# Optimization experiments

Hardware: AMD Instinct MI355X
Metric: run time of the kernel (lower is better)

## Reference

```python
import jax, jax.numpy as jnp
import numpy as np
from jax import lax

F_SIZE = 128
N_HEADS = 8
HEAD_D = F_SIZE // N_HEADS
LANE_F = 64
NUM_PREDS = 6


def _layernorm(x, g, b, eps=1e-5):
    m = x.mean(-1, keepdims=True)
    v = jnp.var(x, axis=-1, keepdims=True)
    return (x - m) * lax.rsqrt(v + eps) * g + b


def _lstm_cell(x, h, c, wih, whh, bih, bhh):
    # PyTorch LSTMCell: gates ordered i, f, g, o
    gates = x @ wih.T + bih + h @ whh.T + bhh
    i, f, g, o = jnp.split(gates, 4, axis=-1)
    c2 = jax.nn.sigmoid(f) * c + jax.nn.sigmoid(i) * jnp.tanh(g)
    h2 = jax.nn.sigmoid(o) * jnp.tanh(c2)
    return h2, c2


def _to_xy(dl, yaw):
    return jnp.concatenate([dl * jnp.cos(yaw), dl * jnp.sin(yaw)], axis=-1)


def _attention(tok_pos, h_ego, h, lane_tok, key_mask, wq, wk, wv, wo, pos_w, pos_b):
    # tokens = [ego, vehicles], keys/values = [tokens, lanes]
    B = h_ego.shape[0]
    tok = jnp.concatenate([h_ego, h], axis=1) + tok_pos @ pos_w + pos_b  # [B,N1,F]
    kv = jnp.concatenate([tok, lane_tok], axis=1)  # [B,N1+L,F]
    q = (tok @ wq).reshape(B, -1, N_HEADS, HEAD_D)
    k = (kv @ wk).reshape(B, -1, N_HEADS, HEAD_D)
    v = (kv @ wv).reshape(B, -1, N_HEADS, HEAD_D)
    s = jnp.einsum('bqhd,bkhd->bhqk', q, k) / jnp.asarray(np.sqrt(HEAD_D), jnp.float32)
    s = jnp.where(key_mask[:, None, None, :] > 0, s, -1e9)
    a = jax.nn.softmax(s, axis=-1)
    o = jnp.einsum('bhqk,bkhd->bqhd', a, v).reshape(B, -1, F_SIZE) @ wo
    tok = tok + o
    return tok[:, :1], tok[:, 1:]


def _forward(input, init_pos, lane_input, mask_input, lane_mask,
             conv_w, conv_b, pos_w, pos_b,
             lane_w1, lane_b1, lane_w2, lane_b2, lane_to_f,
             wq, wk, wv, wo, ln_ego_g, ln_ego_b, ln_g, ln_b,
             ego_wih, ego_whh, ego_bih, ego_bhh,
             veh_wih, veh_whh, veh_bih, veh_bhh,
             out_ego_w, out_ego_b, out_w, out_b, len_pred):
    T, B, N1, _ = input.shape
    V = N1 - 1
    Hh = T - 2  # valid conv over time with kernel 3

    # shared conv_input applied to ego+vehicles at once (same weights in original)
    x = jnp.transpose(input, (1, 3, 2, 0))  # [B,2,N1,T]
    feat = lax.conv_general_dilated(x, conv_w, (1, 1), 'VALID',
                                    dimension_numbers=('NCHW', 'OIHW', 'NCHW'))
    feat = feat + conv_b[None, :, None, None]
    feat = jnp.transpose(feat, (3, 0, 2, 1))  # [Hh,B,N1,F]
    h_ego_seq, h_seq = feat[:, :, :1], feat[:, :, 1:]

    # lane embedding: per-point MLP + mean pool
    lanes = jax.nn.relu(lane_input @ lane_w1 + lane_b1)
    lanes = jax.nn.relu(lanes @ lane_w2 + lane_b2).mean(axis=2)  # [B,L,LANE_F]
    lane_tok = lanes @ lane_to_f  # [B,L,F]
    key_mask = jnp.concatenate([mask_input, lane_mask], axis=1)  # [B,N1+L]

    pos0 = init_pos[0]
    pe0, pv0 = pos0[:, :1], pos0[:, 1:]

    def cell_step(hx_ego, cx_ego, hx, cx, he, hv, pe, pv):
        tok_pos = jnp.concatenate([pe, pv], axis=1)
        ae, av = _attention(tok_pos, he, hv, lane_tok, key_mask, wq, wk, wv, wo, pos_w, pos_b)
        ae = _layernorm(ae.reshape(B, F_SIZE), ln_ego_g, ln_ego_b)
        av = _layernorm(av.reshape(B * V, F_SIZE), ln_g, ln_b)
        hx_ego, cx_ego = _lstm_cell(ae, hx_ego, cx_ego, ego_wih, ego_whh, ego_bih, ego_bhh)
        hx, cx = _lstm_cell(av, hx, cx, veh_wih, veh_whh, veh_bih, veh_bhh)
        return hx_ego, cx_ego, hx, cx

    def hist_step(carry, xs):
        hx_ego, cx_ego, hx, cx, pe, pv = carry
        he, hv, xe, xv = xs
        pe = pe + _to_xy(xe[..., 0:1], xe[..., 1:2])
        pv = pv + _to_xy(xv[..., 0:1], xv[..., 1:2])
        hx_ego, cx_ego, hx, cx = cell_step(hx_ego, cx_ego, hx, cx, he, hv, pe, pv)
        return (hx_ego, cx_ego, hx, cx, pe, pv), None

    carry0 = (jnp.zeros((B, F_SIZE)), jnp.zeros((B, F_SIZE)),
              jnp.zeros((B * V, F_SIZE)), jnp.zeros((B * V, F_SIZE)), pe0, pv0)
    xs = (h_ego_seq, h_seq, input[:Hh, :, :1, :].transpose(0, 1, 2, 3), input[:Hh, :, 1:, :])
    carry, _ = lax.scan(hist_step, carry0, xs)
    hx_ego, cx_ego, hx, cx, pe, pv = carry

    pe = jnp.repeat(pe[:, :, None, :], NUM_PREDS, axis=2)  # [B,1,P,2]
    pv = jnp.repeat(pv[:, :, None, :], NUM_PREDS, axis=2)  # [B,V,P,2]

    def pred_step(carry, _):
        hx_ego, cx_ego, hx, cx, pe, pv = carry
        he = hx_ego.reshape(B, 1, F_SIZE)
        hv = hx.reshape(B, V, F_SIZE)
        hx_ego, cx_ego, hx, cx = cell_step(hx_ego, cx_ego, hx, cx, he, hv,
                                           pe.mean(axis=2), pv.mean(axis=2))
        oe = (hx_ego @ out_ego_w + out_ego_b).reshape(B, 1, NUM_PREDS, 6)
        ov = (hx @ out_w + out_b).reshape(B, V, NUM_PREDS, 6)
        pe = pe + _to_xy(oe[..., 0:1], oe[..., 1:2])
        pv = pv + _to_xy(ov[..., 0:1], ov[..., 1:2])
        y = jnp.concatenate([
            jnp.concatenate([pe, oe[..., 2:6]], axis=-1),
            jnp.concatenate([pv, ov[..., 2:6]], axis=-1)], axis=1)  # [B,N1,P,6]
        return (hx_ego, cx_ego, hx, cx, pe, pv), y

    carry = (hx_ego, cx_ego, hx, cx, pe, pv)
    _, ys = lax.scan(pred_step, carry, None, length=len_pred)
    return ys  # [len_pred,B,N1,NUM_PREDS,6]


def setup_inputs() -> dict:
    key = jax.random.key(0)
    ks = jax.random.split(key, 40)
    B, T, N1, L, PTS = 128, 22, 32, 64, 10
    F, LF, G4, P6 = F_SIZE, LANE_F, 4 * F_SIZE, NUM_PREDS * 6
    s = 0.05
    inp = {}
    inp['input'] = jax.random.normal(ks[0], (T, B, N1, 2), jnp.float32) * 0.1
    inp['init_pos'] = jax.random.normal(ks[1], (1, B, N1, 2), jnp.float32) * 10.0
    inp['lane_input'] = jax.random.normal(ks[2], (B, L, PTS, 2), jnp.float32)
    inp['mask_input'] = jnp.ones((B, N1), jnp.float32)
    inp['lane_mask'] = jnp.ones((B, L), jnp.float32)
    inp['conv_w'] = jax.random.normal(ks[3], (F, 2, 1, 3), jnp.float32) * s
    inp['conv_b'] = jnp.zeros((F,), jnp.float32)
    inp['pos_w'] = jax.random.normal(ks[4], (2, F), jnp.float32) * s
    inp['pos_b'] = jnp.zeros((F,), jnp.float32)
    inp['lane_w1'] = jax.random.normal(ks[5], (2, LF), jnp.float32) * s
    inp['lane_b1'] = jnp.zeros((LF,), jnp.float32)
    inp['lane_w2'] = jax.random.normal(ks[6], (LF, LF), jnp.float32) * s
    inp['lane_b2'] = jnp.zeros((LF,), jnp.float32)
    inp['lane_to_f'] = jax.random.normal(ks[7], (LF, F), jnp.float32) * s
    inp['wq'] = jax.random.normal(ks[8], (F, F), jnp.float32) * s
    inp['wk'] = jax.random.normal(ks[9], (F, F), jnp.float32) * s
    inp['wv'] = jax.random.normal(ks[10], (F, F), jnp.float32) * s
    inp['wo'] = jax.random.normal(ks[11], (F, F), jnp.float32) * s
    inp['ln_ego_g'] = jnp.ones((F,), jnp.float32)
    inp['ln_ego_b'] = jnp.zeros((F,), jnp.float32)
    inp['ln_g'] = jnp.ones((F,), jnp.float32)
    inp['ln_b'] = jnp.zeros((F,), jnp.float32)
    inp['ego_wih'] = jax.random.normal(ks[12], (G4, F), jnp.float32) * s
    inp['ego_whh'] = jax.random.normal(ks[13], (G4, F), jnp.float32) * s
    inp['ego_bih'] = jnp.zeros((G4,), jnp.float32)
    inp['ego_bhh'] = jnp.zeros((G4,), jnp.float32)
    inp['veh_wih'] = jax.random.normal(ks[14], (G4, F), jnp.float32) * s
    inp['veh_whh'] = jax.random.normal(ks[15], (G4, F), jnp.float32) * s
    inp['veh_bih'] = jnp.zeros((G4,), jnp.float32)
    inp['veh_bhh'] = jnp.zeros((G4,), jnp.float32)
    inp['out_ego_w'] = jax.random.normal(ks[16], (F, P6), jnp.float32) * s
    inp['out_ego_b'] = jnp.zeros((P6,), jnp.float32)
    inp['out_w'] = jax.random.normal(ks[17], (F, P6), jnp.float32) * s
    inp['out_b'] = jnp.zeros((P6,), jnp.float32)
    inp['len_pred'] = 30
    return inp


def reference(input, init_pos, lane_input, mask_input, lane_mask,
              conv_w, conv_b, pos_w, pos_b,
              lane_w1, lane_b1, lane_w2, lane_b2, lane_to_f,
              wq, wk, wv, wo, ln_ego_g, ln_ego_b, ln_g, ln_b,
              ego_wih, ego_whh, ego_bih, ego_bhh,
              veh_wih, veh_whh, veh_bih, veh_bhh,
              out_ego_w, out_ego_b, out_w, out_b, len_pred):
    return _forward(input, init_pos, lane_input, mask_input, lane_mask,
                    conv_w, conv_b, pos_w, pos_b,
                    lane_w1, lane_b1, lane_w2, lane_b2, lane_to_f,
                    wq, wk, wv, wo, ln_ego_g, ln_ego_b, ln_g, ln_b,
                    ego_wih, ego_whh, ego_bih, ego_bhh,
                    veh_wih, veh_whh, veh_bih, veh_bhh,
                    out_ego_w, out_ego_b, out_w, out_b, len_pred)
```

## Files before the change

### kernel.cpp

```cpp
#include <hip/hip_runtime.h>
#include <hip/hip_bf16.h>
#include <math.h>

constexpr int B   = 128;
constexpr int N1  = 32;
constexpr int HH  = 20;
constexpr int L   = 64;
constexpr int PTS = 10;
constexpr int F   = 128;
constexpr int LF  = 64;
constexpr int NH  = 8;
constexpr int HD  = 16;
constexpr int KVN = 96;
constexpr int G4  = 512;
constexpr int NP  = 6;
constexpr int P6  = 36;
constexpr int LEN = 30;

__device__ __forceinline__ float sigmoidf(float x) { return 1.f / (1.f + expf(-x)); }
__device__ __forceinline__ float dot4(float4 a, float4 b) {
    return a.x * b.x + a.y * b.y + a.z * b.z + a.w * b.w;
}


__global__ __launch_bounds__(64) void k_lane_tok(
        const float* __restrict__ lane_input,
        const float* __restrict__ w1, const float* __restrict__ b1,
        const float* __restrict__ w2, const float* __restrict__ b2,
        const float* __restrict__ to_f,
        float* __restrict__ kvbuf) {
    int bl = blockIdx.x; int b = bl / L, l = bl % L;
    int j = threadIdx.x;
    __shared__ float w1s[2 * LF];
    __shared__ float b1s[LF];
    __shared__ float ml[LF];
    w1s[j] = w1[j]; w1s[LF + j] = w1[LF + j]; b1s[j] = b1[j];
    float x0[PTS], x1[PTS];
#pragma unroll
    for (int p = 0; p < PTS; ++p) {
        x0[p] = lane_input[((size_t)(b * L + l) * PTS + p) * 2 + 0];
        x1[p] = lane_input[((size_t)(b * L + l) * PTS + p) * 2 + 1];
    }
    __syncthreads();
    float mp[PTS];
#pragma unroll
    for (int p = 0; p < PTS; ++p) mp[p] = 0.f;
    for (int hh = 0; hh < LF; ++hh) {
        float w10 = w1s[hh], w11 = w1s[LF + hh], b1h = b1s[hh];
        float wv = w2[hh * LF + j];
#pragma unroll
        for (int p = 0; p < PTS; ++p) {
            float h1v = fmaxf(x0[p] * w10 + x1[p] * w11 + b1h, 0.f);
            mp[p] += h1v * wv;
        }
    }
    float b2j = b2[j];
    float m = 0.f;
#pragma unroll
    for (int p = 0; p < PTS; ++p) m += fmaxf(mp[p] + b2j, 0.f);
    ml[j] = m * (1.f / PTS);
    __syncthreads();
    float* outp = kvbuf + ((size_t)(b * KVN) + 32 + l) * F;
    float acc0 = 0.f, acc1 = 0.f;
    for (int j2 = 0; j2 < LF; ++j2) {
        float mv = ml[j2];
        acc0 += mv * to_f[j2 * F + j];
        acc1 += mv * to_f[j2 * F + 64 + j];
    }
    outp[j] = acc0; outp[64 + j] = acc1;
}

__global__ __launch_bounds__(256) void k_lane_kv(
        const float* __restrict__ kvbuf,
        const float* __restrict__ wk_t, const float* __restrict__ wv_t,
        float* __restrict__ kb, float* __restrict__ vb) {
    int g = blockIdx.x & 7, b = blockIdx.x >> 3;
    int n0 = 32 + g * 8;
    int tid = threadIdx.x;
    int w = tid >> 6, j = tid & 63;
    int r0 = (w >> 1) * 4;
    int c = (w & 1) * 64 + j;
    __shared__ float tok[8][F];
    for (int i = tid; i < 8 * F; i += 256) {
        int r = i >> 7, cc = i & 127;
        tok[r][cc] = kvbuf[((size_t)b * KVN + n0 + r) * F + cc];
    }
    __syncthreads();
    float ak[4] = {0, 0, 0, 0}, av[4] = {0, 0, 0, 0};
    for (int k2 = 0; k2 < F; k2 += 4) {
        float4 wkv = *(const float4*)(wk_t + (size_t)c * F + k2);
        float4 wvv = *(const float4*)(wv_t + (size_t)c * F + k2);
#pragma unroll
        for (int r = 0; r < 4; ++r) {
            float4 xv = *(const float4*)&tok[r0 + r][k2];
            ak[r] += dot4(xv, wkv); av[r] += dot4(xv, wvv);
        }
    }
#pragma unroll
    for (int r = 0; r < 4; ++r) {
        int n = n0 + r0 + r;
        kb[((size_t)b * KVN + n) * F + c] = ak[r];
        vb[((size_t)b * KVN + n) * F + c] = av[r];
    }
}

__global__ void k_hist_pos(const float* __restrict__ input,
                           const float* __restrict__ init_pos,
                           float* __restrict__ hist_pos,
                           float* __restrict__ pred_pos) {
    int idx = blockIdx.x * blockDim.x + threadIdx.x;
    if (idx >= B * N1) return;
    float px = init_pos[idx * 2], py = init_pos[idx * 2 + 1];
    int b = idx / N1, n = idx % N1;
    for (int t = 0; t < HH; ++t) {
        const float* ip = input + ((size_t)(t * B + b) * N1 + n) * 2;
        float dl = ip[0], yaw = ip[1];
        px += dl * cosf(yaw);
        py += dl * sinf(yaw);
        float* hp = hist_pos + ((size_t)(t * B + b) * N1 + n) * 2;
        hp[0] = px; hp[1] = py;
    }
#pragma unroll
    for (int p = 0; p < NP; ++p) {
        pred_pos[((size_t)idx * NP + p) * 2 + 0] = px;
        pred_pos[((size_t)idx * NP + p) * 2 + 1] = py;
    }
}

__global__ void k_transpose4(const float* __restrict__ w0, const float* __restrict__ w1,
                             const float* __restrict__ w2, const float* __restrict__ w3,
                             float* __restrict__ wt) {
    int m = blockIdx.x >> 7, c = blockIdx.x & 127;
    int k = threadIdx.x;
    const float* src = (m == 0) ? w0 : (m == 1) ? w1 : (m == 2) ? w2 : w3;
    wt[(size_t)m * F * F + (size_t)c * F + k] = src[(size_t)k * F + c];
}

__global__ void k_transpose_lstm(const float* __restrict__ w0, const float* __restrict__ w1,
                                 const float* __restrict__ w2, const float* __restrict__ w3,
                                 float* __restrict__ wt) {
    int m = blockIdx.x >> 7, k = blockIdx.x & 127;
    int f = threadIdx.x;
    const float* src = (m == 0) ? w0 : (m == 1) ? w1 : (m == 2) ? w2 : w3;
    float4 v;
    v.x = src[(size_t)(0 * 128 + f) * F + k];
    v.y = src[(size_t)(1 * 128 + f) * F + k];
    v.z = src[(size_t)(2 * 128 + f) * F + k];
    v.w = src[(size_t)(3 * 128 + f) * F + k];
    *(float4*)(wt + (size_t)m * G4 * F + (size_t)k * G4 + 4 * f) = v;
}


__global__ __launch_bounds__(256) void k_tok_qkv(
        const float* __restrict__ input, const float* __restrict__ hist_pos,
        const float* __restrict__ h, const float* __restrict__ pred_pos,
        const float* __restrict__ conv_w, const float* __restrict__ conv_b,
        const float* __restrict__ pos_w, const float* __restrict__ pos_b,
        const float* __restrict__ wq_t, const float* __restrict__ wk_t,
        const float* __restrict__ wv_t,
        float* __restrict__ kvbuf, float* __restrict__ qb,
        float* __restrict__ kb, float* __restrict__ vb,
        int mode, int t) {
    int g = blockIdx.x & 3, b = blockIdx.x >> 2;
    int n0 = g * 8;
    int tid = threadIdx.x;
    int w = tid >> 6, j = tid & 63;
    int r0 = (w >> 1) * 4;
    int c = (w & 1) * 64 + j;
    __shared__ float tok[8][F];
    __shared__ float mpos[8][2];
    if (mode == 1 && tid < 8) {
        const float* pp = pred_pos + ((size_t)(b * N1 + n0 + tid)) * NP * 2;
        float mx = 0.f, my = 0.f;
#pragma unroll
        for (int p = 0; p < NP; ++p) { mx += pp[p * 2]; my += pp[p * 2 + 1]; }
        mpos[tid][0] = mx * (1.f / NP); mpos[tid][1] = my * (1.f / NP);
    }
    __syncthreads();
    for (int i = tid; i < 8 * F; i += 256) {
        int r = i >> 7, cc = i & 127;
        int n = n0 + r;
        float acc;
        if (mode == 0) {
            acc = conv_b[cc];
#pragma unroll
            for (int kt = 0; kt < 3; ++kt) {
                const float* ip = input + ((size_t)((t + kt) * B + b) * N1 + n) * 2;
                acc += ip[0] * conv_w[(cc * 2 + 0) * 3 + kt] + ip[1] * conv_w[(cc * 2 + 1) * 3 + kt];
            }
            const float* hp = hist_pos + ((size_t)(t * B + b) * N1 + n) * 2;
            acc += hp[0] * pos_w[cc] + hp[1] * pos_w[F + cc] + pos_b[cc];
        } else {
            acc = h[((size_t)b * N1 + n) * F + cc]
                + mpos[r][0] * pos_w[cc] + mpos[r][1] * pos_w[F + cc] + pos_b[cc];
        }
        tok[r][cc] = acc;
        kvbuf[((size_t)b * KVN + n) * F + cc] = acc;
    }
    __syncthreads();
    float aq[4] = {0, 0, 0, 0}, ak[4] = {0, 0, 0, 0}, av[4] = {0, 0, 0, 0};
    for (int k2 = 0; k2 < F; k2 += 4) {
        float4 wqv = *(const float4*)(wq_t + (size_t)c * F + k2);
        float4 wkv = *(const float4*)(wk_t + (size_t)c * F + k2);
        float4 wvv = *(const float4*)(wv_t + (size_t)c * F + k2);
#pragma unroll
        for (int r = 0; r < 4; ++r) {
            float4 xv = *(const float4*)&tok[r0 + r][k2];
            aq[r] += dot4(xv, wqv); ak[r] += dot4(xv, wkv); av[r] += dot4(xv, wvv);
        }
    }
#pragma unroll
    for (int r = 0; r < 4; ++r) {
        int n = n0 + r0 + r;
        qb[((size_t)b * N1 + n) * F + c]  = aq[r];
        kb[((size_t)b * KVN + n) * F + c] = ak[r];
        vb[((size_t)b * KVN + n) * F + c] = av[r];
    }
}

__global__ __launch_bounds__(256) void k_attn(
        const float* __restrict__ qb, const float* __restrict__ kb,
        const float* __restrict__ vb,
        const float* __restrict__ mask_in, const float* __restrict__ lane_mask,
        float* __restrict__ ao) {
    int hb = blockIdx.x & 1, b = blockIdx.x >> 1;
    int tid = threadIdx.x;
    int w = tid >> 6, t = tid & 63;
    int h = hb * 4 + w;
    int qr = t & 31, dh = t >> 5;
    __shared__ float mk[KVN];
    if (tid < KVN)
        mk[tid] = (tid < N1) ? mask_in[b * N1 + tid] : lane_mask[b * L + (tid - N1)];
    const float* qp = qb + ((size_t)b * N1 + qr) * F + h * HD + dh * 8;
    float4 q0 = *(const float4*)qp, q1 = *(const float4*)(qp + 4);
    __syncthreads();
    const float* kbase = kb + (size_t)b * KVN * F + h * HD + dh * 8;
    const float* vbase = vb + (size_t)b * KVN * F + h * HD + dh * 8;
    float mA = -1e30f, lA = 0.f, mB = -1e30f, lB = 0.f;
    float4 oA0 = {0,0,0,0}, oA1 = {0,0,0,0}, oB0 = {0,0,0,0}, oB1 = {0,0,0,0};
    constexpr int HALF = KVN / 2;
    for (int kc = 0; kc < HALF; ++kc) {
        int ka = kc, kb2 = kc + HALF;
        float4 a0 = *(const float4*)(kbase + (size_t)ka * F);
        float4 a1 = *(const float4*)(kbase + (size_t)ka * F + 4);
        float4 b0 = *(const float4*)(kbase + (size_t)kb2 * F);
        float4 b1 = *(const float4*)(kbase + (size_t)kb2 * F + 4);
        float shA = dot4(q0, a0) + dot4(q1, a1);
        float shB = dot4(q0, b0) + dot4(q1, b1);
        float sA = shA + __shfl_xor(shA, 32, 64);
        float sB = shB + __shfl_xor(shB, 32, 64);
        sA = (mk[ka]  > 0.f) ? sA * 0.25f : -1e9f;
        sB = (mk[kb2] > 0.f) ? sB * 0.25f : -1e9f;
        float mnA = fmaxf(mA, sA), mnB = fmaxf(mB, sB);
        float cA = expf(mA - mnA), cB = expf(mB - mnB);
        float pA = expf(sA - mnA), pB = expf(sB - mnB);
        lA = lA * cA + pA; lB = lB * cB + pB;
        float4 va0 = *(const float4*)(vbase + (size_t)ka * F);
        float4 va1 = *(const float4*)(vbase + (size_t)ka * F + 4);
        float4 vb0 = *(const float4*)(vbase + (size_t)kb2 * F);
        float4 vb1 = *(const float4*)(vbase + (size_t)kb2 * F + 4);
        oA0.x = fmaf(oA0.x, cA, pA * va0.x); oA0.y = fmaf(oA0.y, cA, pA * va0.y);
        oA0.z = fmaf(oA0.z, cA, pA * va0.z); oA0.w = fmaf(oA0.w, cA, pA * va0.w);
        oA1.x = fmaf(oA1.x, cA, pA * va1.x); oA1.y = fmaf(oA1.y, cA, pA * va1.y);
        oA1.z = fmaf(oA1.z, cA, pA * va1.z); oA1.w = fmaf(oA1.w, cA, pA * va1.w);
        oB0.x = fmaf(oB0.x, cB, pB * vb0.x); oB0.y = fmaf(oB0.y, cB, pB * vb0.y);
        oB0.z = fmaf(oB0.z, cB, pB * vb0.z); oB0.w = fmaf(oB0.w, cB, pB * vb0.w);
        oB1.x = fmaf(oB1.x, cB, pB * vb1.x); oB1.y = fmaf(oB1.y, cB, pB * vb1.y);
        oB1.z = fmaf(oB1.z, cB, pB * vb1.z); oB1.w = fmaf(oB1.w, cB, pB * vb1.w);
        mA = mnA; mB = mnB;
    }
    float mn = fmaxf(mA, mB);
    float fa = expf(mA - mn), fb = expf(mB - mn);
    float l = lA * fa + lB * fb;
    float inv = 1.f / l;
    float ia = fa * inv, ib = fb * inv;
    float4 o0, o1;
    o0.x = oA0.x * ia + oB0.x * ib; o0.y = oA0.y * ia + oB0.y * ib;
    o0.z = oA0.z * ia + oB0.z * ib; o0.w = oA0.w * ia + oB0.w * ib;
    o1.x = oA1.x * ia + oB1.x * ib; o1.y = oA1.y * ia + oB1.y * ib;
    o1.z = oA1.z * ia + oB1.z * ib; o1.w = oA1.w * ia + oB1.w * ib;
    float* op = ao + ((size_t)b * N1 + qr) * F + h * HD + dh * 8;
    *(float4*)op = o0; *(float4*)(op + 4) = o1;
}

__global__ __launch_bounds__(256) void k_proj_ln(
        const float* __restrict__ ao, const float* __restrict__ kvbuf,
        const float* __restrict__ wo_t,
        const float* __restrict__ ln_ego_g, const float* __restrict__ ln_ego_b,
        const float* __restrict__ ln_g, const float* __restrict__ ln_b,
        float* __restrict__ xln) {
    int gq = blockIdx.x & 3, b = blockIdx.x >> 2;
    int n0 = gq * 8;
    int tid = threadIdx.x;
    int w = tid >> 6, j = tid & 63;
    int r0 = w * 2;
    __shared__ float as[8][F];
    for (int i = tid; i < 8 * F; i += 256) {
        int r = i >> 7, cc = i & 127;
        as[r][cc] = ao[((size_t)b * N1 + n0 + r) * F + cc];
    }
    __syncthreads();
    float acc[2][2] = {{0, 0}, {0, 0}};
    for (int k2 = 0; k2 < F; k2 += 4) {
        float4 w0 = *(const float4*)(wo_t + (size_t)j * F + k2);
        float4 w1 = *(const float4*)(wo_t + (size_t)(j + 64) * F + k2);
#pragma unroll
        for (int r = 0; r < 2; ++r) {
            float4 av4 = *(const float4*)&as[r0 + r][k2];
            acc[r][0] += dot4(av4, w0);
            acc[r][1] += dot4(av4, w1);
        }
    }
#pragma unroll
    for (int r = 0; r < 2; ++r) {
        int n = n0 + r0 + r;
        size_t base = ((size_t)b * KVN + n) * F;
        float x0 = kvbuf[base + j] + acc[r][0];
        float x1 = kvbuf[base + j + 64] + acc[r][1];
        float s1 = x0 + x1, s2 = x0 * x0 + x1 * x1;
#pragma unroll
        for (int off = 32; off > 0; off >>= 1) {
            s1 += __shfl_xor(s1, off, 64);
            s2 += __shfl_xor(s2, off, 64);
        }
        float mean = s1 * (1.f / F);
        float var = s2 * (1.f / F) - mean * mean;
        float rstd = rsqrtf(var + 1e-5f);
        const float* gg = (n == 0) ? ln_ego_g : ln_g;
        const float* bbv = (n == 0) ? ln_ego_b : ln_b;
        size_t ob = ((size_t)b * N1 + n) * F;
        xln[ob + j]      = (x0 - mean) * rstd * gg[j] + bbv[j];
        xln[ob + j + 64] = (x1 - mean) * rstd * gg[j + 64] + bbv[j + 64];
    }
}

__device__ __forceinline__ void lstm_load_w(const float* __restrict__ wi,
                                            const float* __restrict__ wh,
                                            int k4, int ln, float4* wbuf) {
#pragma unroll
    for (int kk = 0; kk < 4; ++kk) {
        const float* pi = wi + (size_t)(k4 + kk) * G4 + 4 * ln;
        const float* ph = wh + (size_t)(k4 + kk) * G4 + 4 * ln;
        wbuf[kk * 4 + 0] = *(const float4*)pi;
        wbuf[kk * 4 + 1] = *(const float4*)(pi + 256);
        wbuf[kk * 4 + 2] = *(const float4*)ph;
        wbuf[kk * 4 + 3] = *(const float4*)(ph + 256);
    }
}

__device__ __forceinline__ void lstm_fma(int k4, int r0,
                                         const float (*xs)[F], const float (*hs)[F],
                                         const float4* wbuf, float (*acc)[8]) {
    float4 xv[4], hv[4];
#pragma unroll
    for (int r = 0; r < 4; ++r) {
        xv[r] = *(const float4*)&xs[r0 + r][k4];
        hv[r] = *(const float4*)&hs[r0 + r][k4];
    }
#pragma unroll
    for (int kk = 0; kk < 4; ++kk) {
        float4 wa0 = wbuf[kk * 4 + 0], wa1 = wbuf[kk * 4 + 1];
        float4 wb0 = wbuf[kk * 4 + 2], wb1 = wbuf[kk * 4 + 3];
#pragma unroll
        for (int r = 0; r < 4; ++r) {
            float x = ((const float*)&xv[r])[kk];
            float hc = ((const float*)&hv[r])[kk];
            acc[r][0] += x * wa0.x + hc * wb0.x;
            acc[r][1] += x * wa0.y + hc * wb0.y;
            acc[r][2] += x * wa0.z + hc * wb0.z;
            acc[r][3] += x * wa0.w + hc * wb0.w;
            acc[r][4] += x * wa1.x + hc * wb1.x;
            acc[r][5] += x * wa1.y + hc * wb1.y;
            acc[r][6] += x * wa1.z + hc * wb1.z;
            acc[r][7] += x * wa1.w + hc * wb1.w;
        }
    }
}

__global__ __launch_bounds__(256, 1) void k_lstm_pred(
        const float* __restrict__ xln,
        const float* __restrict__ ego_wih_t, const float* __restrict__ ego_whh_t,
        const float* __restrict__ ego_bih, const float* __restrict__ ego_bhh,
        const float* __restrict__ veh_wih_t, const float* __restrict__ veh_whh_t,
        const float* __restrict__ veh_bih, const float* __restrict__ veh_bhh,
        const float* __restrict__ h_in, const float* __restrict__ c_in,
        float* __restrict__ h_out, float* __restrict__ c_out,
        const float* __restrict__ out_ego_w, const float* __restrict__ out_ego_b,
        const float* __restrict__ out_w, const float* __restrict__ out_b,
        float* __restrict__ pred_pos, float* __restrict__ out,
        int mode, int step) {
    int n = blockIdx.x >> 3, bg = blockIdx.x & 7;
    int b0 = bg * 16;
    int tid = threadIdx.x;
    int w = tid >> 6, ln = tid & 63;
    int r0 = w * 4;
    const float *wih, *whh, *bih, *bhh;
    if (n == 0) { wih = ego_wih_t; whh = ego_whh_t; bih = ego_bih; bhh = ego_bhh; }
    else        { wih = veh_wih_t; whh = veh_whh_t; bih = veh_bih; bhh = veh_bhh; }
    __shared__ float xs[16][F];
    __shared__ float hs[16][F];
    __shared__ float h2s[16][F];
    __shared__ float os[16][P6];
    for (int i = tid; i < 16 * (F / 4); i += 256) {
        int r = i >> 5, c4 = i & 31;
        size_t bn = (size_t)(b0 + r) * N1 + n;
        *(float4*)&xs[r][c4 * 4] = *(const float4*)(xln  + bn * F + c4 * 4);
        *(float4*)&hs[r][c4 * 4] = *(const float4*)(h_in + bn * F + c4 * 4);
    }
    __syncthreads();
    float acc[4][8];
    {
        float bs[8];
#pragma unroll
        for (int g = 0; g < 4; ++g) {
            bs[g]     = bih[g * 128 + ln]      + bhh[g * 128 + ln];
            bs[4 + g] = bih[g * 128 + 64 + ln] + bhh[g * 128 + 64 + ln];
        }
#pragma unroll
        for (int r = 0; r < 4; ++r)
#pragma unroll
            for (int q = 0; q < 8; ++q) acc[r][q] = bs[q];
    }
    float4 wc[16], wn[16];
    lstm_load_w(wih, whh, 0, ln, wc);
    for (int k4 = 0; k4 < F; k4 += 8) {
        lstm_load_w(wih, whh, k4 + 4, ln, wn);
        lstm_fma(k4, r0, xs, hs, wc, acc);
        if (k4 + 8 < F) lstm_load_w(wih, whh, k4 + 8, ln, wc);
        lstm_fma(k4 + 4, r0, xs, hs, wn, acc);
    }
#pragma unroll
    for (int r = 0; r < 4; ++r) {
        int row = r0 + r;
        size_t bn = (size_t)(b0 + row) * N1 + n;
        float ca = c_in[bn * F + ln];
        float cb2 = c_in[bn * F + 64 + ln];
        float c2a = sigmoidf(acc[r][1]) * ca + sigmoidf(acc[r][0]) * tanhf(acc[r][2]);
        float h2a = sigmoidf(acc[r][3]) * tanhf(c2a);
        float c2b = sigmoidf(acc[r][5]) * cb2 + sigmoidf(acc[r][4]) * tanhf(acc[r][6]);
        float h2b = sigmoidf(acc[r][7]) * tanhf(c2b);
        c_out[bn * F + ln] = c2a;      h_out[bn * F + ln] = h2a;
        c_out[bn * F + 64 + ln] = c2b; h_out[bn * F + 64 + ln] = h2b;
        h2s[row][ln] = h2a;            h2s[row][64 + ln] = h2b;
    }
    if (mode == 1) {
        const float* W  = (n == 0) ? out_ego_w : out_w;
        const float* bb = (n == 0) ? out_ego_b : out_b;
        __syncthreads();
        for (int i = tid; i < 16 * P6; i += 256) {
            int r = i / P6, jo = i % P6;
            float a = bb[jo];
            for (int k4 = 0; k4 < F; k4 += 4) {
                float4 hx = *(const float4*)&h2s[r][k4];
                a += hx.x * W[(k4    ) * P6 + jo] + hx.y * W[(k4 + 1) * P6 + jo]
                   + hx.z * W[(k4 + 2) * P6 + jo] + hx.w * W[(k4 + 3) * P6 + jo];
            }
            os[r][jo] = a;
        }
        __syncthreads();
        if (tid < 16 * NP) {
            int r = tid / NP, p = tid % NP;
            size_t bn = (size_t)(b0 + r) * N1 + n;
            float dl = os[r][p * 6 + 0], yaw = os[r][p * 6 + 1];
            float* pp = pred_pos + (bn * NP + p) * 2;
            float px = pp[0] + dl * cosf(yaw);
            float py = pp[1] + dl * sinf(yaw);
            pp[0] = px; pp[1] = py;
            float* y = out + (size_t)step * B * N1 * P6 + (bn * NP + p) * 6;
            y[0] = px; y[1] = py;
            y[2] = os[r][p * 6 + 2]; y[3] = os[r][p * 6 + 3];
            y[4] = os[r][p * 6 + 4]; y[5] = os[r][p * 6 + 5];
        }
    }
}

extern "C" void kernel_launch(void* const* d_in, const int* in_sizes, int n_in,
                              void* d_out, int out_size, void* d_ws, size_t ws_size,
                              hipStream_t stream) {
    const float* input      = (const float*)d_in[0];
    const float* init_pos   = (const float*)d_in[1];
    const float* lane_input = (const float*)d_in[2];
    const float* mask_input = (const float*)d_in[3];
    const float* lane_mask  = (const float*)d_in[4];
    const float* conv_w     = (const float*)d_in[5];
    const float* conv_b     = (const float*)d_in[6];
    const float* pos_w      = (const float*)d_in[7];
    const float* pos_b      = (const float*)d_in[8];
    const float* lane_w1    = (const float*)d_in[9];
    const float* lane_b1    = (const float*)d_in[10];
    const float* lane_w2    = (const float*)d_in[11];
    const float* lane_b2    = (const float*)d_in[12];
    const float* lane_to_f  = (const float*)d_in[13];
    const float* wq         = (const float*)d_in[14];
    const float* wk         = (const float*)d_in[15];
    const float* wv         = (const float*)d_in[16];
    const float* wo         = (const float*)d_in[17];
    const float* ln_ego_g   = (const float*)d_in[18];
    const float* ln_ego_b   = (const float*)d_in[19];
    const float* ln_g       = (const float*)d_in[20];
    const float* ln_b       = (const float*)d_in[21];
    const float* ego_wih    = (const float*)d_in[22];
    const float* ego_whh    = (const float*)d_in[23];
    const float* ego_bih    = (const float*)d_in[24];
    const float* ego_bhh    = (const float*)d_in[25];
    const float* veh_wih    = (const float*)d_in[26];
    const float* veh_whh    = (const float*)d_in[27];
    const float* veh_bih    = (const float*)d_in[28];
    const float* veh_bhh    = (const float*)d_in[29];
    const float* out_ego_w  = (const float*)d_in[30];
    const float* out_ego_b  = (const float*)d_in[31];
    const float* out_w      = (const float*)d_in[32];
    const float* out_b      = (const float*)d_in[33];

    float* out = (float*)d_out;
    float* ws = (float*)d_ws;

    float* kv       = ws;
    float* qb       = kv + (size_t)B * KVN * F;
    float* kb       = qb + (size_t)B * N1 * F;
    float* vb       = kb + (size_t)B * KVN * F;
    float* ao       = vb + (size_t)B * KVN * F;
    float* xln      = ao + (size_t)B * N1 * F;
    float* h0       = xln + (size_t)B * N1 * F;
    float* h1p      = h0 + (size_t)B * N1 * F;
    float* c0       = h1p + (size_t)B * N1 * F;
    float* c1p      = c0 + (size_t)B * N1 * F;
    float* hist_pos = c1p + (size_t)B * N1 * F;
    float* pred_pos = hist_pos + (size_t)HH * B * N1 * 2;
    float* wqkvo_t  = pred_pos + (size_t)B * N1 * NP * 2;
    float* wq_t = wqkvo_t;
    float* wk_t = wqkvo_t + (size_t)F * F;
    float* wv_t = wqkvo_t + (size_t)2 * F * F;
    float* wo_t = wqkvo_t + (size_t)3 * F * F;
    float* wlstm_t  = wqkvo_t + (size_t)4 * F * F;
    float* ego_wih_t = wlstm_t;
    float* ego_whh_t = wlstm_t + (size_t)G4 * F;
    float* veh_wih_t = wlstm_t + (size_t)2 * G4 * F;
    float* veh_whh_t = wlstm_t + (size_t)3 * G4 * F;

    float* hb[2] = {h0, h1p};
    float* cb[2] = {c0, c1p};

    hipMemsetAsync(h0, 0, (size_t)B * N1 * F * sizeof(float), stream);
    hipMemsetAsync(c0, 0, (size_t)B * N1 * F * sizeof(float), stream);
    k_transpose4<<<4 * F, F, 0, stream>>>(wq, wk, wv, wo, wqkvo_t);
    k_transpose_lstm<<<4 * F, F, 0, stream>>>(ego_wih, ego_whh, veh_wih, veh_whh, wlstm_t);
    k_lane_tok<<<B * L, 64, 0, stream>>>(lane_input, lane_w1, lane_b1, lane_w2, lane_b2,
                                         lane_to_f, kv);
    k_hist_pos<<<(B * N1 + 255) / 256, 256, 0, stream>>>(input, init_pos, hist_pos, pred_pos);
    k_lane_kv<<<B * 8, 256, 0, stream>>>(kv, wk_t, wv_t, kb, vb);

    int cur = 0;
    for (int step = 0; step < HH + LEN; ++step) {
        int mode = (step < HH) ? 0 : 1;
        int t = (mode == 0) ? step : 0;
        int s = (mode == 0) ? 0 : step - HH;
        k_tok_qkv<<<B * 4, 256, 0, stream>>>(input, hist_pos, hb[cur], pred_pos,
                                             conv_w, conv_b, pos_w, pos_b,
                                             wq_t, wk_t, wv_t, kv, qb, kb, vb, mode, t);
        k_attn<<<B * 2, 256, 0, stream>>>(qb, kb, vb, mask_input, lane_mask, ao);
        k_proj_ln<<<B * 4, 256, 0, stream>>>(ao, kv, wo_t, ln_ego_g, ln_ego_b, ln_g, ln_b, xln);
        k_lstm_pred<<<N1 * 8, 256, 0, stream>>>(xln, ego_wih_t, ego_whh_t, ego_bih, ego_bhh,
                                                veh_wih_t, veh_whh_t, veh_bih, veh_bhh,
                                                hb[cur], cb[cur], hb[1 - cur], cb[1 - cur],
                                                out_ego_w, out_ego_b, out_w, out_b,
                                                pred_pos, out, mode, s);
        cur ^= 1;
    }
}
```

Measured before the change: 6.618 ms.

## Fuse output projection and layernorm into LSTM kernel, split ih/hh across waves

Merges the per-step output-projection+layernorm kernel into the LSTM kernel, removing one launch per step and the xln global round trip. The LSTM matmul is restructured so one wave handles the input weights and another the recurrent weights for 8 rows each, with partial gate sums combined through shared memory. Gate biases are pre-summed once into a reordered buffer. Blocks now have 128 threads over 512 blocks, and the wo projection is recomputed per (n, batch group) tile, which may change occupancy and latency hiding.

```diff
diff --git a/kernel.cpp b/kernel.cpp
--- a/kernel.cpp
+++ b/kernel.cpp
@@ -148,6 +148,16 @@
     v.z = src[(size_t)(2 * 128 + f) * F + k];
     v.w = src[(size_t)(3 * 128 + f) * F + k];
     *(float4*)(wt + (size_t)m * G4 * F + (size_t)k * G4 + 4 * f) = v;
+}
+
+__global__ void k_prep_bias(const float* __restrict__ bih_e, const float* __restrict__ bhh_e,
+                            const float* __restrict__ bih_v, const float* __restrict__ bhh_v,
+                            float* __restrict__ bsum) {
+    int m = blockIdx.x; int ci = threadIdx.x;
+    int f = ci >> 2, g = ci & 3;
+    const float* bi = m ? bih_v : bih_e;
+    const float* bh = m ? bhh_v : bhh_e;
+    bsum[m * G4 + ci] = bi[g * 128 + f] + bh[g * 128 + f];
 }
 
 
@@ -283,182 +293,166 @@
     *(float4*)op = o0; *(float4*)(op + 4) = o1;
 }
 
-__global__ __launch_bounds__(256) void k_proj_ln(
+__device__ __forceinline__ void lstm_fma4(const float (*xs)[F], int k4,
+                                          const float4* wb, float (*acc)[8]) {
+#pragma unroll
+    for (int r = 0; r < 8; ++r) {
+        float4 xv = *(const float4*)&xs[r][k4];
+        const float* xf = (const float*)&xv;
+#pragma unroll
+        for (int kk = 0; kk < 4; ++kk) {
+            float x = xf[kk];
+            float4 wA = wb[kk * 2], wB = wb[kk * 2 + 1];
+            acc[r][0] += x * wA.x; acc[r][1] += x * wA.y;
+            acc[r][2] += x * wA.z; acc[r][3] += x * wA.w;
+            acc[r][4] += x * wB.x; acc[r][5] += x * wB.y;
+            acc[r][6] += x * wB.z; acc[r][7] += x * wB.w;
+        }
+    }
+}
+
+__global__ __launch_bounds__(128, 1) void k_proj_lstm(
         const float* __restrict__ ao, const float* __restrict__ kvbuf,
         const float* __restrict__ wo_t,
         const float* __restrict__ ln_ego_g, const float* __restrict__ ln_ego_b,
         const float* __restrict__ ln_g, const float* __restrict__ ln_b,
-        float* __restrict__ xln) {
-    int gq = blockIdx.x & 3, b = blockIdx.x >> 2;
-    int n0 = gq * 8;
-    int tid = threadIdx.x;
-    int w = tid >> 6, j = tid & 63;
-    int r0 = w * 2;
-    __shared__ float as[8][F];
-    for (int i = tid; i < 8 * F; i += 256) {
-        int r = i >> 7, cc = i & 127;
-        as[r][cc] = ao[((size_t)b * N1 + n0 + r) * F + cc];
-    }
-    __syncthreads();
-    float acc[2][2] = {{0, 0}, {0, 0}};
-    for (int k2 = 0; k2 < F; k2 += 4) {
-        float4 w0 = *(const float4*)(wo_t + (size_t)j * F + k2);
-        float4 w1 = *(const float4*)(wo_t + (size_t)(j + 64) * F + k2);
-#pragma unroll
-        for (int r = 0; r < 2; ++r) {
-            float4 av4 = *(const float4*)&as[r0 + r][k2];
-            acc[r][0] += dot4(av4, w0);
-            acc[r][1] += dot4(av4, w1);
-        }
-    }
-#pragma unroll
-    for (int r = 0; r < 2; ++r) {
-        int n = n0 + r0 + r;
-        size_t base = ((size_t)b * KVN + n) * F;
-        float x0 = kvbuf[base + j] + acc[r][0];
-        float x1 = kvbuf[base + j + 64] + acc[r][1];
-        float s1 = x0 + x1, s2 = x0 * x0 + x1 * x1;
-#pragma unroll
-        for (int off = 32; off > 0; off >>= 1) {
-            s1 += __shfl_xor(s1, off, 64);
-            s2 += __shfl_xor(s2, off, 64);
-        }
-        float mean = s1 * (1.f / F);
-        float var = s2 * (1.f / F) - mean * mean;
-        float rstd = rsqrtf(var + 1e-5f);
-        const float* gg = (n == 0) ? ln_ego_g : ln_g;
-        const float* bbv = (n == 0) ? ln_ego_b : ln_b;
-        size_t ob = ((size_t)b * N1 + n) * F;
-        xln[ob + j]      = (x0 - mean) * rstd * gg[j] + bbv[j];
-        xln[ob + j + 64] = (x1 - mean) * rstd * gg[j + 64] + bbv[j + 64];
-    }
-}
-
-__device__ __forceinline__ void lstm_load_w(const float* __restrict__ wi,
-                                            const float* __restrict__ wh,
-                                            int k4, int ln, float4* wbuf) {
-#pragma unroll
-    for (int kk = 0; kk < 4; ++kk) {
-        const float* pi = wi + (size_t)(k4 + kk) * G4 + 4 * ln;
-        const float* ph = wh + (size_t)(k4 + kk) * G4 + 4 * ln;
-        wbuf[kk * 4 + 0] = *(const float4*)pi;
-        wbuf[kk * 4 + 1] = *(const float4*)(pi + 256);
-        wbuf[kk * 4 + 2] = *(const float4*)ph;
-        wbuf[kk * 4 + 3] = *(const float4*)(ph + 256);
-    }
-}
-
-__device__ __forceinline__ void lstm_fma(int k4, int r0,
-                                         const float (*xs)[F], const float (*hs)[F],
-                                         const float4* wbuf, float (*acc)[8]) {
-    float4 xv[4], hv[4];
-#pragma unroll
-    for (int r = 0; r < 4; ++r) {
-        xv[r] = *(const float4*)&xs[r0 + r][k4];
-        hv[r] = *(const float4*)&hs[r0 + r][k4];
-    }
-#pragma unroll
-    for (int kk = 0; kk < 4; ++kk) {
-        float4 wa0 = wbuf[kk * 4 + 0], wa1 = wbuf[kk * 4 + 1];
-        float4 wb0 = wbuf[kk * 4 + 2], wb1 = wbuf[kk * 4 + 3];
-#pragma unroll
-        for (int r = 0; r < 4; ++r) {
-            float x = ((const float*)&xv[r])[kk];
-            float hc = ((const float*)&hv[r])[kk];
-            acc[r][0] += x * wa0.x + hc * wb0.x;
-            acc[r][1] += x * wa0.y + hc * wb0.y;
-            acc[r][2] += x * wa0.z + hc * wb0.z;
-            acc[r][3] += x * wa0.w + hc * wb0.w;
-            acc[r][4] += x * wa1.x + hc * wb1.x;
-            acc[r][5] += x * wa1.y + hc * wb1.y;
-            acc[r][6] += x * wa1.z + hc * wb1.z;
-            acc[r][7] += x * wa1.w + hc * wb1.w;
-        }
-    }
-}
-
-__global__ __launch_bounds__(256, 1) void k_lstm_pred(
-        const float* __restrict__ xln,
         const float* __restrict__ ego_wih_t, const float* __restrict__ ego_whh_t,
-        const float* __restrict__ ego_bih, const float* __restrict__ ego_bhh,
         const float* __restrict__ veh_wih_t, const float* __restrict__ veh_whh_t,
-        const float* __restrict__ veh_bih, const float* __restrict__ veh_bhh,
+        const float* __restrict__ bsum_all,
         const float* __restrict__ h_in, const float* __restrict__ c_in,
         float* __restrict__ h_out, float* __restrict__ c_out,
         const float* __restrict__ out_ego_w, const float* __restrict__ out_ego_b,
         const float* __restrict__ out_w, const float* __restrict__ out_b,
         float* __restrict__ pred_pos, float* __restrict__ out,
         int mode, int step) {
-    int n = blockIdx.x >> 3, bg = blockIdx.x & 7;
-    int b0 = bg * 16;
+    int n = blockIdx.x >> 4, bg = blockIdx.x & 15;
+    int b0 = bg * 8;
     int tid = threadIdx.x;
-    int w = tid >> 6, ln = tid & 63;
-    int r0 = w * 4;
-    const float *wih, *whh, *bih, *bhh;
-    if (n == 0) { wih = ego_wih_t; whh = ego_whh_t; bih = ego_bih; bhh = ego_bhh; }
-    else        { wih = veh_wih_t; whh = veh_whh_t; bih = veh_bih; bhh = veh_bhh; }
-    __shared__ float xs[16][F];
-    __shared__ float hs[16][F];
-    __shared__ float h2s[16][F];
-    __shared__ float os[16][P6];
-    for (int i = tid; i < 16 * (F / 4); i += 256) {
-        int r = i >> 5, c4 = i & 31;
+    int w = tid >> 6, j = tid & 63;
+    __shared__ float as_[8][F];
+    __shared__ float xh[2][8][F];
+    __shared__ float gacc[2][8][G4];
+    __shared__ float h2s[8][F];
+    __shared__ float os[8][P6];
+    for (int i = tid; i < 8 * (F / 4); i += 128) {
+        int r = i >> 5, c4 = (i & 31) * 4;
         size_t bn = (size_t)(b0 + r) * N1 + n;
-        *(float4*)&xs[r][c4 * 4] = *(const float4*)(xln  + bn * F + c4 * 4);
-        *(float4*)&hs[r][c4 * 4] = *(const float4*)(h_in + bn * F + c4 * 4);
-    }
-    __syncthreads();
-    float acc[4][8];
+        *(float4*)&as_[r][c4]   = *(const float4*)(ao   + bn * F + c4);
+        *(float4*)&xh[1][r][c4] = *(const float4*)(h_in + bn * F + c4);
+    }
+    __syncthreads();
     {
-        float bs[8];
-#pragma unroll
-        for (int g = 0; g < 4; ++g) {
-            bs[g]     = bih[g * 128 + ln]      + bhh[g * 128 + ln];
-            bs[4 + g] = bih[g * 128 + 64 + ln] + bhh[g * 128 + 64 + ln];
-        }
-#pragma unroll
-        for (int r = 0; r < 4; ++r)
-#pragma unroll
-            for (int q = 0; q < 8; ++q) acc[r][q] = bs[q];
-    }
-    float4 wc[16], wn[16];
-    lstm_load_w(wih, whh, 0, ln, wc);
-    for (int k4 = 0; k4 < F; k4 += 8) {
-        lstm_load_w(wih, whh, k4 + 4, ln, wn);
-        lstm_fma(k4, r0, xs, hs, wc, acc);
-        if (k4 + 8 < F) lstm_load_w(wih, whh, k4 + 8, ln, wc);
-        lstm_fma(k4 + 4, r0, xs, hs, wn, acc);
-    }
-#pragma unroll
-    for (int r = 0; r < 4; ++r) {
-        int row = r0 + r;
-        size_t bn = (size_t)(b0 + row) * N1 + n;
-        float ca = c_in[bn * F + ln];
-        float cb2 = c_in[bn * F + 64 + ln];
-        float c2a = sigmoidf(acc[r][1]) * ca + sigmoidf(acc[r][0]) * tanhf(acc[r][2]);
-        float h2a = sigmoidf(acc[r][3]) * tanhf(c2a);
-        float c2b = sigmoidf(acc[r][5]) * cb2 + sigmoidf(acc[r][4]) * tanhf(acc[r][6]);
-        float h2b = sigmoidf(acc[r][7]) * tanhf(c2b);
-        c_out[bn * F + ln] = c2a;      h_out[bn * F + ln] = h2a;
-        c_out[bn * F + 64 + ln] = c2b; h_out[bn * F + 64 + ln] = h2b;
-        h2s[row][ln] = h2a;            h2s[row][64 + ln] = h2b;
+        int r0 = w * 4;
+        float a0[4] = {0, 0, 0, 0}, a1[4] = {0, 0, 0, 0};
+        for (int k4 = 0; k4 < F; k4 += 4) {
+            float4 w0 = *(const float4*)(wo_t + (size_t)j * F + k4);
+            float4 w1 = *(const float4*)(wo_t + (size_t)(j + 64) * F + k4);
+#pragma unroll
+            for (int r = 0; r < 4; ++r) {
+                float4 av = *(const float4*)&as_[r0 + r][k4];
+                a0[r] += dot4(av, w0); a1[r] += dot4(av, w1);
+            }
+        }
+        const float* gg  = (n == 0) ? ln_ego_g : ln_g;
+        const float* bbv = (n == 0) ? ln_ego_b : ln_b;
+        float g0 = gg[j], g1 = gg[j + 64], bb0 = bbv[j], bb1 = bbv[j + 64];
+#pragma unroll
+        for (int r = 0; r < 4; ++r) {
+            int b = b0 + r0 + r;
+            size_t base = ((size_t)b * KVN + n) * F;
+            float x0 = kvbuf[base + j] + a0[r];
+            float x1 = kvbuf[base + j + 64] + a1[r];
+            float s1 = x0 + x1, s2 = x0 * x0 + x1 * x1;
+#pragma unroll
+            for (int off = 32; off > 0; off >>= 1) {
+                s1 += __shfl_xor(s1, off, 64);
+                s2 += __shfl_xor(s2, off, 64);
+            }
+            float mean = s1 * (1.f / F);
+            float var = s2 * (1.f / F) - mean * mean;
+            float rstd = rsqrtf(var + 1e-5f);
+            xh[0][r0 + r][j]      = (x0 - mean) * rstd * g0 + bb0;
+            xh[0][r0 + r][j + 64] = (x1 - mean) * rstd * g1 + bb1;
+        }
+    }
+    __syncthreads();
+    const float* W = (n == 0) ? (w == 0 ? ego_wih_t : ego_whh_t)
+                              : (w == 0 ? veh_wih_t : veh_whh_t);
+    const float* Wp = W + 8 * j;
+    const float (*xsrc)[F] = xh[w];
+    float acc[8][8];
+    if (w == 0) {
+        const float* bsum = bsum_all + (n == 0 ? 0 : G4);
+        float4 bv0 = *(const float4*)(bsum + 8 * j);
+        float4 bv1 = *(const float4*)(bsum + 8 * j + 4);
+#pragma unroll
+        for (int r = 0; r < 8; ++r) {
+            acc[r][0] = bv0.x; acc[r][1] = bv0.y; acc[r][2] = bv0.z; acc[r][3] = bv0.w;
+            acc[r][4] = bv1.x; acc[r][5] = bv1.y; acc[r][6] = bv1.z; acc[r][7] = bv1.w;
+        }
+    } else {
+#pragma unroll
+        for (int r = 0; r < 8; ++r)
+#pragma unroll
+            for (int q = 0; q < 8; ++q) acc[r][q] = 0.f;
+    }
+    float4 wc[8], wn[8];
+#pragma unroll
+    for (int kk = 0; kk < 4; ++kk) {
+        wc[kk * 2]     = *(const float4*)(Wp + (size_t)kk * G4);
+        wc[kk * 2 + 1] = *(const float4*)(Wp + (size_t)kk * G4 + 4);
+    }
+    for (int k8 = 0; k8 < F; k8 += 8) {
+#pragma unroll
+        for (int kk = 0; kk < 4; ++kk) {
+            wn[kk * 2]     = *(const float4*)(Wp + (size_t)(k8 + 4 + kk) * G4);
+            wn[kk * 2 + 1] = *(const float4*)(Wp + (size_t)(k8 + 4 + kk) * G4 + 4);
+        }
+        lstm_fma4(xsrc, k8, wc, acc);
+        if (k8 + 8 < F) {
+#pragma unroll
+            for (int kk = 0; kk < 4; ++kk) {
+                wc[kk * 2]     = *(const float4*)(Wp + (size_t)(k8 + 8 + kk) * G4);
+                wc[kk * 2 + 1] = *(const float4*)(Wp + (size_t)(k8 + 8 + kk) * G4 + 4);
+            }
+        }
+        lstm_fma4(xsrc, k8 + 4, wn, acc);
+    }
+#pragma unroll
+    for (int r = 0; r < 8; ++r) {
+        *(float4*)&gacc[w][r][8 * j]     = make_float4(acc[r][0], acc[r][1], acc[r][2], acc[r][3]);
+        *(float4*)&gacc[w][r][8 * j + 4] = make_float4(acc[r][4], acc[r][5], acc[r][6], acc[r][7]);
+    }
+    __syncthreads();
+#pragma unroll
+    for (int r = 0; r < 8; ++r) {
+        float4 gx = *(const float4*)&gacc[0][r][4 * tid];
+        float4 gh = *(const float4*)&gacc[1][r][4 * tid];
+        float ig = gx.x + gh.x, fg = gx.y + gh.y, gg = gx.z + gh.z, og = gx.w + gh.w;
+        size_t bn = (size_t)(b0 + r) * N1 + n;
+        float cold = c_in[bn * F + tid];
+        float c2 = sigmoidf(fg) * cold + sigmoidf(ig) * tanhf(gg);
+        float h2 = sigmoidf(og) * tanhf(c2);
+        c_out[bn * F + tid] = c2;
+        h_out[bn * F + tid] = h2;
+        h2s[r][tid] = h2;
     }
     if (mode == 1) {
-        const float* W  = (n == 0) ? out_ego_w : out_w;
+        const float* Wo = (n == 0) ? out_ego_w : out_w;
         const float* bb = (n == 0) ? out_ego_b : out_b;
         __syncthreads();
-        for (int i = tid; i < 16 * P6; i += 256) {
+        for (int i = tid; i < 8 * P6; i += 128) {
             int r = i / P6, jo = i % P6;
             float a = bb[jo];
             for (int k4 = 0; k4 < F; k4 += 4) {
                 float4 hx = *(const float4*)&h2s[r][k4];
-                a += hx.x * W[(k4    ) * P6 + jo] + hx.y * W[(k4 + 1) * P6 + jo]
-                   + hx.z * W[(k4 + 2) * P6 + jo] + hx.w * W[(k4 + 3) * P6 + jo];
+                a += hx.x * Wo[(k4    ) * P6 + jo] + hx.y * Wo[(k4 + 1) * P6 + jo]
+                   + hx.z * Wo[(k4 + 2) * P6 + jo] + hx.w * Wo[(k4 + 3) * P6 + jo];
             }
             os[r][jo] = a;
         }
         __syncthreads();
-        if (tid < 16 * NP) {
+        if (tid < 8 * NP) {
             int r = tid / NP, p = tid % NP;
             size_t bn = (size_t)(b0 + r) * N1 + n;
             float dl = os[r][p * 6 + 0], yaw = os[r][p * 6 + 1];
@@ -520,8 +514,7 @@
     float* kb       = qb + (size_t)B * N1 * F;
     float* vb       = kb + (size_t)B * KVN * F;
     float* ao       = vb + (size_t)B * KVN * F;
-    float* xln      = ao + (size_t)B * N1 * F;
-    float* h0       = xln + (size_t)B * N1 * F;
+    float* h0       = ao + (size_t)B * N1 * F;
     float* h1p      = h0 + (size_t)B * N1 * F;
     float* c0       = h1p + (size_t)B * N1 * F;
     float* c1p      = c0 + (size_t)B * N1 * F;
@@ -537,6 +530,7 @@
     float* ego_whh_t = wlstm_t + (size_t)G4 * F;
     float* veh_wih_t = wlstm_t + (size_t)2 * G4 * F;
     float* veh_whh_t = wlstm_t + (size_t)3 * G4 * F;
+    float* bsum_all  = wlstm_t + (size_t)4 * G4 * F;
 
     float* hb[2] = {h0, h1p};
     float* cb[2] = {c0, c1p};
@@ -545,6 +539,7 @@
     hipMemsetAsync(c0, 0, (size_t)B * N1 * F * sizeof(float), stream);
     k_transpose4<<<4 * F, F, 0, stream>>>(wq, wk, wv, wo, wqkvo_t);
     k_transpose_lstm<<<4 * F, F, 0, stream>>>(ego_wih, ego_whh, veh_wih, veh_whh, wlstm_t);
+    k_prep_bias<<<2, G4, 0, stream>>>(ego_bih, ego_bhh, veh_bih, veh_bhh, bsum_all);
     k_lane_tok<<<B * L, 64, 0, stream>>>(lane_input, lane_w1, lane_b1, lane_w2, lane_b2,
                                          lane_to_f, kv);
     k_hist_pos<<<(B * N1 + 255) / 256, 256, 0, stream>>>(input, init_pos, hist_pos, pred_pos);
@@ -559,12 +554,13 @@
                                              conv_w, conv_b, pos_w, pos_b,
                                              wq_t, wk_t, wv_t, kv, qb, kb, vb, mode, t);
         k_attn<<<B * 2, 256, 0, stream>>>(qb, kb, vb, mask_input, lane_mask, ao);
-        k_proj_ln<<<B * 4, 256, 0, stream>>>(ao, kv, wo_t, ln_ego_g, ln_ego_b, ln_g, ln_b, xln);
-        k_lstm_pred<<<N1 * 8, 256, 0, stream>>>(xln, ego_wih_t, ego_whh_t, ego_bih, ego_bhh,
-                                                veh_wih_t, veh_whh_t, veh_bih, veh_bhh,
-                                                hb[cur], cb[cur], hb[1 - cur], cb[1 - cur],
-                                                out_ego_w, out_ego_b, out_w, out_b,
-                                                pred_pos, out, mode, s);
+        k_proj_lstm<<<N1 * 16, 128, 0, stream>>>(ao, kv, wo_t,
+                                                 ln_ego_g, ln_ego_b, ln_g, ln_b,
+                                                 ego_wih_t, ego_whh_t, veh_wih_t, veh_whh_t,
+                                                 bsum_all,
+                                                 hb[cur], cb[cur], hb[1 - cur], cb[1 - cur],
+                                                 out_ego_w, out_ego_b, out_w, out_b,
+                                                 pred_pos, out, mode, s);
         cur ^= 1;
     }
 }
```

Result: faster. 6.183 ms (-6.6%).
